# Performance work log

Hardware: AMD Instinct MI355X
Metric: run time of the kernel (lower is better)

The kernel has to match this reference:

```python
import jax, jax.numpy as jnp
import numpy as np

B, S, D, H, L, FF, V, TYPES = 16, 512, 1024, 16, 8, 4096, 30522, 2
DH = D // H
BETA = 1.0          # pbit_temperature
EPS = 1e-12         # layer_norm_eps
STD = 0.02          # initializer_range


def _ln(x, g, b):
    m = x.mean(-1, keepdims=True)
    v = ((x - m) ** 2).mean(-1, keepdims=True)
    return (x - m) * jax.lax.rsqrt(v + EPS) * g + b


def setup_inputs() -> dict:
    key = jax.random.key(0)
    ks = iter(jax.random.split(key, 32))
    rn = lambda shape: (jax.random.normal(next(ks), shape, dtype=jnp.float32) * STD)
    inp = {
        'input_ids': jax.random.randint(next(ks), (B, S), 0, V),
        'token_type_ids': jax.random.randint(next(ks), (B, S), 0, TYPES),
        'tok_emb': rn((V, D)),
        'pos_emb': rn((S, D)),
        'type_emb': rn((TYPES, D)),
        'emb_g': jnp.ones((D,), jnp.float32),
        'emb_b': jnp.zeros((D,), jnp.float32),
        # stacked per-layer parameters [L, ...]
        'Wq': rn((L, D, D)), 'bq': jnp.zeros((L, D), jnp.float32),
        'Wk': rn((L, D, D)), 'bk': jnp.zeros((L, D), jnp.float32),
        'Wv': rn((L, D, D)), 'bv': jnp.zeros((L, D), jnp.float32),
        'Wo': rn((L, D, D)), 'bo': jnp.zeros((L, D), jnp.float32),
        'ln1_g': jnp.ones((L, D), jnp.float32), 'ln1_b': jnp.zeros((L, D), jnp.float32),
        'ln2_g': jnp.ones((L, D), jnp.float32), 'ln2_b': jnp.zeros((L, D), jnp.float32),
        'W1': rn((L, D, FF)), 'b1': jnp.zeros((L, FF), jnp.float32),
        'W2': rn((L, FF, D)), 'b2': jnp.zeros((L, D), jnp.float32),
    }
    return inp


def reference(input_ids, token_type_ids, tok_emb, pos_emb, type_emb, emb_g, emb_b,
              Wq, bq, Wk, bk, Wv, bv, Wo, bo, ln1_g, ln1_b, ln2_g, ln2_b,
              W1, b1, W2, b2):
    # Embeddings (eval mode: TSU noise + dropout are identity)
    h = tok_emb[input_ids] + pos_emb[None, :, :] + type_emb[token_type_ids]
    h = _ln(h, emb_g, emb_b)

    def layer(h, p):
        wq, bq_, wk, bk_, wv, bv_, wo, bo_, g1, bb1, g2, bb2, w1, bf1, w2, bf2 = p
        x = _ln(h, g1, bb1)  # pre-LN per TinyBioBERTLayer
        q = (x @ wq + bq_).reshape(B, S, H, DH)
        k = (x @ wk + bk_).reshape(B, S, H, DH)
        v = (x @ wv + bv_).reshape(B, S, H, DH)
        # P-bit attention in expectation == temperature-scaled softmax SDPA
        scores = jnp.einsum('bqhd,bkhd->bhqk', q, k) * (BETA / np.sqrt(DH))
        a = jax.nn.softmax(scores, axis=-1)
        ctx = jnp.einsum('bhqk,bkhd->bqhd', a, v).reshape(B, S, D)
        h = h + ctx @ wo + bo_
        y = _ln(h, g2, bb2)
        y = jax.nn.gelu(y @ w1 + bf1, approximate=False) @ w2 + bf2
        return h + y, None

    params = (Wq, bq, Wk, bk, Wv, bv, Wo, bo, ln1_g, ln1_b, ln2_g, ln2_b, W1, b1, W2, b2)
    h, _ = jax.lax.scan(layer, h, params)
    return h
```

## Files before the change

kernel.cpp:

```cpp
#include <hip/hip_runtime.h>
#include <math.h>

#define B_  16
#define S_  512
#define D_  1024
#define H_  16
#define DH_ 64
#define L_  8
#define FF_ 4096
#define M_  (B_*S_)

typedef __attribute__((ext_vector_type(4))) float  f32x4;
typedef __attribute__((ext_vector_type(8))) short  s8v;
typedef __attribute__((ext_vector_type(4))) short  s4v;
typedef __attribute__((ext_vector_type(8))) __bf16 bf8v;

__device__ __forceinline__ short f2bf(float f) {
  union { float f; unsigned u; } x; x.f = f;
  unsigned r = x.u + 0x7fffu + ((x.u >> 16) & 1u);
  return (short)(r >> 16);
}

__device__ __forceinline__ f32x4 mfma16(s8v a, s8v b, f32x4 c) {
  return __builtin_amdgcn_mfma_f32_16x16x32_bf16(
      __builtin_bit_cast(bf8v, a), __builtin_bit_cast(bf8v, b), c, 0, 0, 0);
}

__device__ __forceinline__ void gl_lds16(const void* g, void* lds) {
  __builtin_amdgcn_global_load_lds(
      (const __attribute__((address_space(1))) unsigned int*)g,
      (__attribute__((address_space(3))) unsigned int*)lds, 16, 0, 0);
}

__device__ __forceinline__ float gelu_f(float v) {
  const float t  = 0.7978845608f * (v + 0.044715f * v * v * v);
  const float e  = __expf(-2.0f * fabsf(t));
  const float th = copysignf((1.f - e) / (1.f + e), t);
  return 0.5f * v * (1.0f + th);
}

__global__ __launch_bounds__(256) void tcvt(const float* __restrict__ src,
                                            short* __restrict__ dst, int R, int C,
                                            size_t dls) {
  __shared__ float tile[32][33];
  src += (size_t)blockIdx.z * R * C;
  dst += (size_t)blockIdx.z * dls;
  const int c0 = blockIdx.x * 32, r0 = blockIdx.y * 32;
  const int tx = threadIdx.x & 31, ty = threadIdx.x >> 5;
#pragma unroll
  for (int i = 0; i < 32; i += 8)
    tile[ty + i][tx] = src[(size_t)(r0 + ty + i) * C + (c0 + tx)];
  __syncthreads();
#pragma unroll
  for (int i = 0; i < 32; i += 8)
    dst[(size_t)(c0 + ty + i) * R + (r0 + tx)] = f2bf(tile[tx][ty + i]);
}

__global__ __launch_bounds__(256) void embed_ln(
    const int* __restrict__ ids, const int* __restrict__ tts,
    const float* __restrict__ tok, const float* __restrict__ pos,
    const float* __restrict__ typ, const float* __restrict__ g,
    const float* __restrict__ bta, float* __restrict__ h) {
  const int row = blockIdx.x;
  const int s = row & (S_ - 1);
  const int id = ids[row], tt = tts[row];
  const int t = threadIdx.x;
  const float4 a = ((const float4*)(tok + (size_t)id * D_))[t];
  const float4 p = ((const float4*)(pos + (size_t)s  * D_))[t];
  const float4 y = ((const float4*)(typ + (size_t)tt * D_))[t];
  float x0 = a.x + p.x + y.x, x1 = a.y + p.y + y.y;
  float x2 = a.z + p.z + y.z, x3 = a.w + p.w + y.w;
  float sum = x0 + x1 + x2 + x3;
  float sq  = x0*x0 + x1*x1 + x2*x2 + x3*x3;
  __shared__ float red[8];
#pragma unroll
  for (int d = 1; d < 64; d <<= 1) { sum += __shfl_xor(sum, d); sq += __shfl_xor(sq, d); }
  if ((t & 63) == 0) { red[t >> 6] = sum; red[(t >> 6) + 4] = sq; }
  __syncthreads();
  sum = red[0] + red[1] + red[2] + red[3];
  sq  = red[4] + red[5] + red[6] + red[7];
  const float mean = sum * (1.f / D_);
  const float var  = sq * (1.f / D_) - mean * mean;
  const float rstd = rsqrtf(fmaxf(var, 0.f) + 1e-12f);
  const float4 gg = ((const float4*)g)[t];
  const float4 bb = ((const float4*)bta)[t];
  float4 o;
  o.x = (x0 - mean) * rstd * gg.x + bb.x;
  o.y = (x1 - mean) * rstd * gg.y + bb.y;
  o.z = (x2 - mean) * rstd * gg.z + bb.z;
  o.w = (x3 - mean) * rstd * gg.w + bb.w;
  ((float4*)(h + (size_t)row * D_))[t] = o;
}

__global__ __launch_bounds__(256) void ln_bf16(
    const float* __restrict__ h, const float* __restrict__ g,
    const float* __restrict__ bta, short* __restrict__ out) {
  const int row = blockIdx.x;
  const int t = threadIdx.x;
  const float4 x = ((const float4*)(h + (size_t)row * D_))[t];
  float sum = x.x + x.y + x.z + x.w;
  float sq  = x.x*x.x + x.y*x.y + x.z*x.z + x.w*x.w;
  __shared__ float red[8];
#pragma unroll
  for (int d = 1; d < 64; d <<= 1) { sum += __shfl_xor(sum, d); sq += __shfl_xor(sq, d); }
  if ((t & 63) == 0) { red[t >> 6] = sum; red[(t >> 6) + 4] = sq; }
  __syncthreads();
  sum = red[0] + red[1] + red[2] + red[3];
  sq  = red[4] + red[5] + red[6] + red[7];
  const float mean = sum * (1.f / D_);
  const float var  = sq * (1.f / D_) - mean * mean;
  const float rstd = rsqrtf(fmaxf(var, 0.f) + 1e-12f);
  const float4 gg = ((const float4*)g)[t];
  const float4 bb = ((const float4*)bta)[t];
  s4v o;
  o[0] = f2bf((x.x - mean) * rstd * gg.x + bb.x);
  o[1] = f2bf((x.y - mean) * rstd * gg.y + bb.y);
  o[2] = f2bf((x.z - mean) * rstd * gg.z + bb.z);
  o[3] = f2bf((x.w - mean) * rstd * gg.w + bb.w);
  *(s4v*)&out[(size_t)row * D_ + t * 4] = o;
}

__global__ __launch_bounds__(256) void ln_red(
    float* __restrict__ h, const float* __restrict__ p0,
    const float* __restrict__ p1, const float* __restrict__ badd,
    const float* __restrict__ g, const float* __restrict__ bta,
    short* __restrict__ out) {
  const int row = blockIdx.x;
  const int t = threadIdx.x;
  const size_t off = (size_t)row * D_;
  float4 x = ((const float4*)(h + off))[t];
  const float4 a = ((const float4*)(p0 + off))[t];
  const float4 b = ((const float4*)(p1 + off))[t];
  const float4 c = ((const float4*)badd)[t];
  x.x += a.x + b.x + c.x; x.y += a.y + b.y + c.y;
  x.z += a.z + b.z + c.z; x.w += a.w + b.w + c.w;
  ((float4*)(h + off))[t] = x;
  float sum = x.x + x.y + x.z + x.w;
  float sq  = x.x*x.x + x.y*x.y + x.z*x.z + x.w*x.w;
  __shared__ float red[8];
#pragma unroll
  for (int d = 1; d < 64; d <<= 1) { sum += __shfl_xor(sum, d); sq += __shfl_xor(sq, d); }
  if ((t & 63) == 0) { red[t >> 6] = sum; red[(t >> 6) + 4] = sq; }
  __syncthreads();
  sum = red[0] + red[1] + red[2] + red[3];
  sq  = red[4] + red[5] + red[6] + red[7];
  const float mean = sum * (1.f / D_);
  const float var  = sq * (1.f / D_) - mean * mean;
  const float rstd = rsqrtf(fmaxf(var, 0.f) + 1e-12f);
  const float4 gg = ((const float4*)g)[t];
  const float4 bb = ((const float4*)bta)[t];
  s4v o;
  o[0] = f2bf((x.x - mean) * rstd * gg.x + bb.x);
  o[1] = f2bf((x.y - mean) * rstd * gg.y + bb.y);
  o[2] = f2bf((x.z - mean) * rstd * gg.z + bb.z);
  o[3] = f2bf((x.w - mean) * rstd * gg.w + bb.w);
  *(s4v*)&out[off + t * 4] = o;
}

__global__ __launch_bounds__(256) void final_add(
    float* __restrict__ h, const float* __restrict__ p0,
    const float* __restrict__ p1, const float* __restrict__ badd) {
  const int row = blockIdx.x;
  const int t = threadIdx.x;
  const size_t off = (size_t)row * D_;
  float4 x = ((const float4*)(h + off))[t];
  const float4 a = ((const float4*)(p0 + off))[t];
  const float4 b = ((const float4*)(p1 + off))[t];
  const float4 c = ((const float4*)badd)[t];
  x.x += a.x + b.x + c.x; x.y += a.y + b.y + c.y;
  x.z += a.z + b.z + c.z; x.w += a.w + b.w + c.w;
  ((float4*)(h + off))[t] = x;
}

template<int MODE>
__global__ __launch_bounds__(512, 1) void gemm8(
    const short* __restrict__ A, const short* __restrict__ Bt,
    const float* __restrict__ b0, const float* __restrict__ b1,
    const float* __restrict__ b2, short* __restrict__ out,
    float* __restrict__ hres, int N, int K, int LD, int nby) {
  __shared__ __align__(16) char lds[131072];
  const int tid = threadIdx.x, wid = tid >> 6, lane = tid & 63;
  const int wr = wid >> 2, wc = wid & 3;
  const int l15 = lane & 15, l4 = lane >> 4;

  const int n8 = (int)gridDim.x >> 3;
  const int bid = (int)blockIdx.x;
  const int xcd = bid & 7, tt_ = bid >> 3;
  const int nbv = (MODE == 4) ? nby * 2 : nby;
  const int cpx = n8 / nbv;
  const int bx = xcd * cpx + tt_ / nbv;
  const int bv = tt_ % nbv;
  const int by = (MODE == 4) ? (bv & 3) : bv;
  const int slice = (MODE == 4) ? (bv >> 2) : 0;
  const int which = (MODE == 6) ? (by >> 2) : 0;

  const short* __restrict__ Ab = A + (size_t)bx * 256 * LD + (size_t)slice * K;
  const short* __restrict__ Bb = Bt + (size_t)by * 256 * LD + (size_t)slice * K;

  const int str0 = tid >> 3;
  const int stc  = (((tid & 7) ^ (str0 & 7)) * 8);
  const int r7  = l15 & 7;
  const int kx0 = ((l4) ^ r7) * 16;
  const int kx1 = ((4 + l4) ^ r7) * 16;
  const int arow = (wr * 128 + l15) * 128;
  const int brow = (wc * 64 + l15) * 128;

  f32x4 acc[8][4];
#pragma unroll
  for (int m = 0; m < 8; ++m)
#pragma unroll
    for (int n = 0; n < 4; ++n) acc[m][n] = f32x4{0.f, 0.f, 0.f, 0.f};
  s8v af[8][2], bf[4][2];

  const int nt = K >> 6, it = nt >> 1;

#define BAR_ __builtin_amdgcn_s_barrier()
#define LGKM0_ asm volatile("s_waitcnt lgkmcnt(0)" ::: "memory")
#define VMC_(n) asm volatile("s_waitcnt vmcnt(" #n ")" ::: "memory")
#define ST_(isB, slot, hh, kt) do { \
    const short* _g = ((isB) ? Bb : Ab) + (size_t)((hh) * 128 + str0) * LD + ((kt) << 6) + stc; \
    char* _d = lds + ((isB) ? 65536 : 0) + (slot) * 32768 + (hh) * 16384 + wid * 1024; \
    gl_lds16(_g, _d); \
    gl_lds16(_g + (size_t)64 * LD, _d + 8192); \
  } while (0)
#define RDA4_(slot, g) do { \
    const char* _p = lds + (slot) * 32768 + arow + (g) * 8192; \
    _Pragma("unroll") for (int _i = 0; _i < 4; ++_i) { \
      af[(g)*4+_i][0] = *(const s8v*)(_p + _i * 2048 + kx0); \
      af[(g)*4+_i][1] = *(const s8v*)(_p + _i * 2048 + kx1); } \
  } while (0)
#define RDB2_(slot, g) do { \
    const char* _p = lds + 65536 + (slot) * 32768 + brow + (g) * 4096; \
    _Pragma("unroll") for (int _i = 0; _i < 2; ++_i) { \
      bf[(g)*2+_i][0] = *(const s8v*)(_p + _i * 2048 + kx0); \
      bf[(g)*2+_i][1] = *(const s8v*)(_p + _i * 2048 + kx1); } \
  } while (0)
#define MM_S(mq, nq) do { \
    __builtin_amdgcn_s_setprio(1); \
    _Pragma("unroll") for (int _mf = 0; _mf < 4; ++_mf) \
    _Pragma("unroll") for (int _nf = 0; _nf < 2; ++_nf) \
    _Pragma("unroll") for (int _ks = 0; _ks < 2; ++_ks) \
      acc[(mq)*4+_mf][(nq)*2+_nf] = \
        mfma16(bf[(nq)*2+_nf][_ks], af[(mq)*4+_mf][_ks], acc[(mq)*4+_mf][(nq)*2+_nf]); \
    __builtin_amdgcn_s_setprio(0); \
  } while (0)
#define MM_U(mq, nq) do { \
    __builtin_amdgcn_s_setprio(1); \
    _Pragma("unroll") for (int _mf = 0; _mf < 4; ++_mf) \
    _Pragma("unroll") for (int _nf = 0; _nf < 2; ++_nf) \
    _Pragma("unroll") for (int _ks = 0; _ks < 2; ++_ks) \
      acc[(mq)*4+_mf][(nq)*2+_nf] = \
        mfma16(af[(mq)*4+_mf][_ks], bf[(nq)*2+_nf][_ks], acc[(mq)*4+_mf][(nq)*2+_nf]); \
    __builtin_amdgcn_s_setprio(0); \
  } while (0)
#define KLOOP_(MMX) \
  for (int t = 0; t < it; ++t) { \
    const int ka = 2 * t, kb = ka + 1; \
    const bool s2 = (ka + 2) < nt, s3 = (kb + 2) < nt; \
    RDA4_(0, 0); RDB2_(0, 0); \
    ST_(1, 1, 1, kb); \
    BAR_; LGKM0_; MMX(0, 0); BAR_; \
    RDB2_(0, 1); \
    BAR_; LGKM0_; MMX(0, 1); BAR_; \
    RDA4_(0, 1); \
    if (s2) ST_(1, 0, 0, ka + 2); \
    BAR_; LGKM0_; MMX(1, 0); BAR_; \
    if (s2) { ST_(1, 0, 1, ka + 2); VMC_(4); } else { VMC_(0); } \
    BAR_; MMX(1, 1); BAR_; \
    RDA4_(1, 0); RDB2_(1, 0); \
    if (s2) ST_(0, 0, 0, ka + 2); \
    BAR_; LGKM0_; MMX(0, 0); BAR_; \
    RDB2_(1, 1); \
    if (s2) ST_(0, 0, 1, ka + 2); \
    BAR_; LGKM0_; MMX(0, 1); BAR_; \
    RDA4_(1, 1); \
    if (s3) ST_(1, 1, 0, kb + 2); \
    BAR_; LGKM0_; MMX(1, 0); BAR_; \
    if (s3) { ST_(0, 1, 0, kb + 2); ST_(0, 1, 1, kb + 2); VMC_(6); } \
    BAR_; MMX(1, 1); BAR_; \
  }

  ST_(1,0,0,0); ST_(1,0,1,0); ST_(0,0,0,0); ST_(0,0,1,0);
  ST_(1,1,0,1); ST_(0,1,0,1); ST_(0,1,1,1);
  VMC_(6);
  BAR_;

  if (MODE == 6 && which == 2) { KLOOP_(MM_U); }
  else                         { KLOOP_(MM_S); }

  const int r0 = bx * 256 + wr * 128;
  const int c0 = by * 256 + wc * 64;
  if (MODE == 6 && which == 2) {
    short* __restrict__ vout = out + 2 * (size_t)M_ * D_;
#pragma unroll
    for (int n = 0; n < 4; ++n) {
      const int col = c0 + n * 16 + l15;
      const int colw = col & (D_ - 1);
      const int hd = colw >> 6, dh = colw & 63;
      const float bb = b2[colw];
#pragma unroll
      for (int m = 0; m < 8; ++m) {
        const int row = r0 + m * 16 + l4 * 4;
        const int b = row >> 9, s = row & 511;
        s4v pk;
#pragma unroll
        for (int rr = 0; rr < 4; ++rr) pk[rr] = f2bf(acc[m][n][rr] + bb);
        *(s4v*)&vout[(((size_t)(b * H_ + hd) * DH_) + dh) * S_ + s] = pk;
      }
    }
    return;
  }
  const float* __restrict__ bias = (MODE == 6) ? (which == 0 ? b0 : b1) : b0;
  short* __restrict__ outw = (MODE == 6) ? out + (size_t)which * M_ * D_ : out;
  float* __restrict__ pp =
      (MODE == 4) ? hres + (size_t)slice * ((size_t)M_ * D_) : hres;

  float4 bb4[4];
#pragma unroll
  for (int n = 0; n < 4; ++n) {
    const int colb = c0 + n * 16 + l4 * 4;
    const int colw = colb & (D_ - 1);
    bb4[n] = float4{0.f, 0.f, 0.f, 0.f};
    if (MODE == 6)              bb4[n] = *(const float4*)&bias[colw];
    else if (MODE != 4 && bias) bb4[n] = *(const float4*)&bias[colb];
  }
#pragma unroll
  for (int m = 0; m < 8; ++m) {
    const int row = r0 + m * 16 + l15;
#pragma unroll
    for (int n = 0; n < 4; ++n) {
      const int colb = c0 + n * 16 + l4 * 4;
      const int colw = colb & (D_ - 1);
      float v0 = acc[m][n][0] + bb4[n].x, v1 = acc[m][n][1] + bb4[n].y;
      float v2 = acc[m][n][2] + bb4[n].z, v3 = acc[m][n][3] + bb4[n].w;
      if (MODE == 2) {
        float4* hp = (float4*)&hres[(size_t)row * N + colb];
        float4 hv = *hp;
        hv.x += v0; hv.y += v1; hv.z += v2; hv.w += v3;
        *hp = hv;
      } else if (MODE == 4) {
        float4 pv; pv.x = v0; pv.y = v1; pv.z = v2; pv.w = v3;
        *(float4*)&pp[(size_t)row * N + colb] = pv;
      } else {
        if (MODE == 1) { v0 = gelu_f(v0); v1 = gelu_f(v1); v2 = gelu_f(v2); v3 = gelu_f(v3); }
        s4v pk;
        pk[0] = f2bf(v0); pk[1] = f2bf(v1); pk[2] = f2bf(v2); pk[3] = f2bf(v3);
        if (MODE == 6) {
          const int b = row >> 9, s = row & 511, hd = colw >> 6, dh = colw & 63;
          *(s4v*)&outw[((((size_t)b * H_ + hd) * S_ + s) << 6) + dh] = pk;
        } else {
          *(s4v*)&outw[(size_t)row * N + colb] = pk;
        }
      }
    }
  }
#undef BAR_
#undef LGKM0_
#undef VMC_
#undef ST_
#undef RDA4_
#undef RDB2_
#undef MM_S
#undef MM_U
#undef KLOOP_
}

__global__ __launch_bounds__(256, 4) void attn(
    const short* __restrict__ Q, const short* __restrict__ K,
    const short* __restrict__ Vt, short* __restrict__ ctx) {
  __shared__ __align__(16) short Kl[64 * 72];
  __shared__ __align__(16) short Vl[64 * 72];
  __shared__ __align__(16) short Pl[4][32 * 72];

  const int tid = threadIdx.x, wid = tid >> 6, lane = tid & 63;
  const int l15 = lane & 15, l4 = lane >> 4;
  const int bid = (int)blockIdx.x;
  const int xcd = bid & 7, idx = bid >> 3;
  const int bh   = xcd * 32 + (idx >> 2);
  const int qblk = idx & 3;
  const short* Qb = Q  + (size_t)bh * S_ * DH_;
  const short* Kb = K  + (size_t)bh * S_ * DH_;
  const short* Vb = Vt + (size_t)bh * DH_ * S_;

  const int qoff = qblk * 128 + wid * 32;

  s8v qf[2][2];
#pragma unroll
  for (int mf = 0; mf < 2; ++mf)
#pragma unroll
    for (int ks = 0; ks < 2; ++ks)
      qf[mf][ks] = *(const s8v*)&Qb[(size_t)(qoff + mf * 16 + l15) * DH_ + ks * 32 + l4 * 8];

  f32x4 o[2][4];
  float rm[2][4], rs[2][4];
#pragma unroll
  for (int mf = 0; mf < 2; ++mf) {
#pragma unroll
    for (int nf = 0; nf < 4; ++nf) o[mf][nf] = f32x4{0.f, 0.f, 0.f, 0.f};
#pragma unroll
    for (int r = 0; r < 4; ++r) { rm[mf][r] = -1e30f; rs[mf][r] = 0.f; }
  }

  const int srow = tid >> 3;
  const int sch  = (tid & 7) * 8;

  s8v rk[2], rv[2];
#pragma unroll
  for (int r = 0; r < 2; ++r) {
    rk[r] = *(const s8v*)&Kb[(size_t)(srow + r * 32) * DH_ + sch];
    rv[r] = *(const s8v*)&Vb[(size_t)(srow + r * 32) * S_ + sch];
  }

  for (int kt = 0; kt < S_ / 64; ++kt) {
    __syncthreads();
#pragma unroll
    for (int r = 0; r < 2; ++r) {
      *(s8v*)&Kl[(srow + r * 32) * 72 + sch] = rk[r];
      *(s8v*)&Vl[(srow + r * 32) * 72 + sch] = rv[r];
    }
    __syncthreads();
    if (kt + 1 < S_ / 64) {
#pragma unroll
      for (int r = 0; r < 2; ++r) {
        rk[r] = *(const s8v*)&Kb[(size_t)((kt + 1) * 64 + srow + r * 32) * DH_ + sch];
        rv[r] = *(const s8v*)&Vb[(size_t)(srow + r * 32) * S_ + (kt + 1) * 64 + sch];
      }
    }

    f32x4 sc[2][4];
#pragma unroll
    for (int mf = 0; mf < 2; ++mf)
#pragma unroll
      for (int nt = 0; nt < 4; ++nt) sc[mf][nt] = f32x4{0.f, 0.f, 0.f, 0.f};
    __builtin_amdgcn_s_setprio(1);
#pragma unroll
    for (int nt = 0; nt < 4; ++nt)
#pragma unroll
      for (int ks = 0; ks < 2; ++ks) {
        const s8v kf = *(const s8v*)&Kl[(nt * 16 + l15) * 72 + ks * 32 + l4 * 8];
#pragma unroll
        for (int mf = 0; mf < 2; ++mf)
          sc[mf][nt] = mfma16(qf[mf][ks], kf, sc[mf][nt]);
      }
    __builtin_amdgcn_s_setprio(0);

#pragma unroll
    for (int mf = 0; mf < 2; ++mf) {
      float tm[4];
#pragma unroll
      for (int r = 0; r < 4; ++r) {
        sc[mf][0][r] *= 0.125f; sc[mf][1][r] *= 0.125f;
        sc[mf][2][r] *= 0.125f; sc[mf][3][r] *= 0.125f;
        tm[r] = fmaxf(fmaxf(sc[mf][0][r], sc[mf][1][r]),
                      fmaxf(sc[mf][2][r], sc[mf][3][r]));
      }
#pragma unroll
      for (int d = 1; d < 16; d <<= 1)
#pragma unroll
        for (int r = 0; r < 4; ++r) tm[r] = fmaxf(tm[r], __shfl_xor(tm[r], d));
      float ps[4];
#pragma unroll
      for (int r = 0; r < 4; ++r) {
        const float nm = fmaxf(rm[mf][r], tm[r]);
        const float so = __expf(rm[mf][r] - nm);
        rm[mf][r] = nm;
        rs[mf][r] *= so;
#pragma unroll
        for (int nf = 0; nf < 4; ++nf) o[mf][nf][r] *= so;
        float psum = 0.f;
#pragma unroll
        for (int nt = 0; nt < 4; ++nt) {
          const float pv = __expf(sc[mf][nt][r] - nm);
          sc[mf][nt][r] = pv;
          psum += pv;
        }
        ps[r] = psum;
      }
#pragma unroll
      for (int d = 1; d < 16; d <<= 1)
#pragma unroll
        for (int r = 0; r < 4; ++r) ps[r] += __shfl_xor(ps[r], d);
#pragma unroll
      for (int r = 0; r < 4; ++r) rs[mf][r] += ps[r];
#pragma unroll
      for (int nt = 0; nt < 4; ++nt)
#pragma unroll
        for (int r = 0; r < 4; ++r)
          Pl[wid][(mf * 16 + l4 * 4 + r) * 72 + nt * 16 + l15] = f2bf(sc[mf][nt][r]);
    }
    asm volatile("s_waitcnt lgkmcnt(0)" ::: "memory");

    __builtin_amdgcn_s_setprio(1);
#pragma unroll
    for (int ks = 0; ks < 2; ++ks) {
      s8v pf[2], vf[4];
#pragma unroll
      for (int mf = 0; mf < 2; ++mf)
        pf[mf] = *(const s8v*)&Pl[wid][(mf * 16 + l15) * 72 + ks * 32 + l4 * 8];
#pragma unroll
      for (int nf = 0; nf < 4; ++nf)
        vf[nf] = *(const s8v*)&Vl[(nf * 16 + l15) * 72 + ks * 32 + l4 * 8];
#pragma unroll
      for (int mf = 0; mf < 2; ++mf)
#pragma unroll
        for (int nf = 0; nf < 4; ++nf)
          o[mf][nf] = mfma16(pf[mf], vf[nf], o[mf][nf]);
    }
    __builtin_amdgcn_s_setprio(0);
  }

  const int bb = bh >> 4, hh = bh & 15;
#pragma unroll
  for (int mf = 0; mf < 2; ++mf)
#pragma unroll
    for (int r = 0; r < 4; ++r) {
      const int qrow = qoff + mf * 16 + l4 * 4 + r;
      const float inv = 1.0f / rs[mf][r];
      short* dst = ctx + (size_t)(bb * S_ + qrow) * D_ + hh * DH_;
#pragma unroll
      for (int nf = 0; nf < 4; ++nf)
        dst[nf * 16 + l15] = f2bf(o[mf][nf][r] * inv);
    }
}

extern "C" void kernel_launch(void* const* d_in, const int* in_sizes, int n_in,
                              void* d_out, int out_size, void* d_ws, size_t ws_size,
                              hipStream_t stream) {
  const int*   ids = (const int*)d_in[0];
  const int*   tts = (const int*)d_in[1];
  const float* tok = (const float*)d_in[2];
  const float* pos = (const float*)d_in[3];
  const float* typ = (const float*)d_in[4];
  const float* eg  = (const float*)d_in[5];
  const float* eb  = (const float*)d_in[6];
  const float* Wq  = (const float*)d_in[7];  const float* bq = (const float*)d_in[8];
  const float* Wk  = (const float*)d_in[9];  const float* bk = (const float*)d_in[10];
  const float* Wv  = (const float*)d_in[11]; const float* bv = (const float*)d_in[12];
  const float* Wo  = (const float*)d_in[13]; const float* bo = (const float*)d_in[14];
  const float* g1  = (const float*)d_in[15]; const float* be1 = (const float*)d_in[16];
  const float* g2  = (const float*)d_in[17]; const float* be2 = (const float*)d_in[18];
  const float* W1  = (const float*)d_in[19]; const float* b1 = (const float*)d_in[20];
  const float* W2  = (const float*)d_in[21]; const float* b2 = (const float*)d_in[22];

  float* h = (float*)d_out;

  const size_t szDD  = (size_t)D_ * D_;
  const size_t szDF  = (size_t)D_ * FF_;
  const size_t xb_b  = (size_t)M_ * D_ * 2;
  const size_t big_b = (size_t)M_ * FF_ * 2;
  const size_t pa_b  = (size_t)M_ * D_ * 4;
  const size_t wfull = (szDD * 4 + szDF * 2) * 2 * L_;
  const bool full = ws_size >= wfull + xb_b + big_b + 8192;
  const bool sk   = ws_size >= wfull + xb_b + big_b + 2 * pa_b + 8192;

  char* p = (char*)d_ws;
  auto alloc = [&](size_t bytes) { char* r = p; p += (bytes + 255) & ~(size_t)255; return r; };
  const size_t wl = full ? L_ : 1;
  short* wqkvT = (short*)alloc(szDD * 3 * 2 * wl);
  short* woT   = (short*)alloc(szDD * 2 * wl);
  short* w1T   = (short*)alloc(szDF * 2 * wl);
  short* w2T   = (short*)alloc(szDF * 2 * wl);
  short* xb  = (short*)alloc(xb_b);
  char*  big = alloc(big_b);
  float* pa0 = sk ? (float*)alloc(pa_b) : nullptr;
  float* pa1 = sk ? (float*)alloc(pa_b) : nullptr;
  short* qb  = (short*)big;
  short* vb  = (short*)(big + 2 * xb_b);
  short* cb  = xb;
  short* tb  = (short*)big;

  if (full) {
    tcvt<<<dim3(D_/32,  D_/32,  L_), 256, 0, stream>>>(Wq, wqkvT,          D_,  D_,  3*szDD);
    tcvt<<<dim3(D_/32,  D_/32,  L_), 256, 0, stream>>>(Wk, wqkvT +   szDD, D_,  D_,  3*szDD);
    tcvt<<<dim3(D_/32,  D_/32,  L_), 256, 0, stream>>>(Wv, wqkvT + 2*szDD, D_,  D_,  3*szDD);
    tcvt<<<dim3(D_/32,  D_/32,  L_), 256, 0, stream>>>(Wo, woT, D_,  D_,  szDD);
    tcvt<<<dim3(FF_/32, D_/32,  L_), 256, 0, stream>>>(W1, w1T, D_,  FF_, szDF);
    tcvt<<<dim3(D_/32,  FF_/32, L_), 256, 0, stream>>>(W2, w2T, FF_, D_,  szDF);
  }

  embed_ln<<<M_, 256, 0, stream>>>(ids, tts, tok, pos, typ, eg, eb, h);

  const int nbx = M_ / 256;
  for (int l = 0; l < L_; ++l) {
    if (!full) {
      tcvt<<<dim3(D_/32,  D_/32,  1), 256, 0, stream>>>(Wq + (size_t)l*szDD, wqkvT,          D_,  D_,  0);
      tcvt<<<dim3(D_/32,  D_/32,  1), 256, 0, stream>>>(Wk + (size_t)l*szDD, wqkvT +   szDD, D_,  D_,  0);
      tcvt<<<dim3(D_/32,  D_/32,  1), 256, 0, stream>>>(Wv + (size_t)l*szDD, wqkvT + 2*szDD, D_,  D_,  0);
      tcvt<<<dim3(D_/32,  D_/32,  1), 256, 0, stream>>>(Wo + (size_t)l*szDD, woT, D_,  D_,  0);
      tcvt<<<dim3(FF_/32, D_/32,  1), 256, 0, stream>>>(W1 + (size_t)l*szDF, w1T, D_,  FF_, 0);
      tcvt<<<dim3(D_/32,  FF_/32, 1), 256, 0, stream>>>(W2 + (size_t)l*szDF, w2T, FF_, D_,  0);
    }
    const size_t o3 = full ? (size_t)l * 3 * szDD : 0;
    const size_t od = full ? (size_t)l * szDD : 0;
    const size_t of = full ? (size_t)l * szDF : 0;

    if (l == 0 || !sk)
      ln_bf16<<<M_, 256, 0, stream>>>(h, g1 + l*D_, be1 + l*D_, xb);
    else
      ln_red<<<M_, 256, 0, stream>>>(h, pa0, pa1, b2 + (l-1)*D_,
                                     g1 + l*D_, be1 + l*D_, xb);

    gemm8<6><<<nbx * (3*D_/256), 512, 0, stream>>>(
        xb, wqkvT + o3, bq + l*D_, bk + l*D_, bv + l*D_, qb, nullptr, 3*D_, D_, D_, 3*D_/256);

    attn<<<(S_/128) * B_ * H_, 256, 0, stream>>>(
        qb, qb + (size_t)M_*D_, vb, cb);

    if (sk) {
      gemm8<4><<<nbx * (D_/256) * 2, 512, 0, stream>>>(
          cb, woT + od, nullptr, nullptr, nullptr, nullptr, pa0, D_, D_/2, D_, D_/256);
      ln_red<<<M_, 256, 0, stream>>>(h, pa0, pa1, bo + l*D_,
                                     g2 + l*D_, be2 + l*D_, xb);
    } else {
      gemm8<2><<<nbx * (D_/256), 512, 0, stream>>>(
          cb, woT + od, bo + l*D_, nullptr, nullptr, nullptr, h, D_, D_, D_, D_/256);
      ln_bf16<<<M_, 256, 0, stream>>>(h, g2 + l*D_, be2 + l*D_, xb);
    }

    gemm8<1><<<nbx * (FF_/256), 512, 0, stream>>>(
        xb, w1T + of, b1 + l*FF_, nullptr, nullptr, tb, nullptr, FF_, D_, D_, FF_/256);

    if (sk) {
      gemm8<4><<<nbx * (D_/256) * 2, 512, 0, stream>>>(
          tb, w2T + of, nullptr, nullptr, nullptr, nullptr, pa0, D_, FF_/2, FF_, D_/256);
    } else {
      gemm8<2><<<nbx * (D_/256), 512, 0, stream>>>(
          tb, w2T + of, b2 + l*D_, nullptr, nullptr, nullptr, h, D_, FF_, FF_, D_/256);
    }
  }
  if (sk)
    final_add<<<M_, 256, 0, stream>>>(h, pa0, pa1, b2 + (L_-1)*D_);
}
```

Baseline: 3.006 ms.

## Switch GEMM to 4 waves with 128x128 per-wave tiles

Reworks the 256x256-tile bf16 GEMM from 8 waves (2x4, 128x64 per wave) to 4 waves (2x2, 128x128 per wave). Each wave now holds 64 accumulator fragments and reuses every A and B fragment read from LDS across more MFMAs, which cuts LDS read traffic per FLOP. Each thread issues twice as many global-to-LDS loads, and the vmcnt waits and the pipeline schedule are adjusted to match. The cost is much higher register pressure (256 accumulator VGPRs plus operands), possible spills, and half as many waves per CU to hide latency.

Measured after the change: 3.965 ms. 1.32x slower.

```diff
diff --git a/kernel.cpp b/kernel.cpp
--- a/kernel.cpp
+++ b/kernel.cpp
@@ -173,14 +173,14 @@
 }
 
 template<int MODE>
-__global__ __launch_bounds__(512, 1) void gemm8(
+__global__ __launch_bounds__(256, 1) void gemm8(
     const short* __restrict__ A, const short* __restrict__ Bt,
     const float* __restrict__ b0, const float* __restrict__ b1,
     const float* __restrict__ b2, short* __restrict__ out,
     float* __restrict__ hres, int N, int K, int LD, int nby) {
   __shared__ __align__(16) char lds[131072];
   const int tid = threadIdx.x, wid = tid >> 6, lane = tid & 63;
-  const int wr = wid >> 2, wc = wid & 3;
+  const int wr = wid >> 1, wc = wid & 1;
   const int l15 = lane & 15, l4 = lane >> 4;
 
   const int n8 = (int)gridDim.x >> 3;
@@ -203,14 +203,14 @@
   const int kx0 = ((l4) ^ r7) * 16;
   const int kx1 = ((4 + l4) ^ r7) * 16;
   const int arow = (wr * 128 + l15) * 128;
-  const int brow = (wc * 64 + l15) * 128;
-
-  f32x4 acc[8][4];
+  const int brow = (wc * 128 + l15) * 128;
+
+  f32x4 acc[8][8];
 #pragma unroll
   for (int m = 0; m < 8; ++m)
 #pragma unroll
-    for (int n = 0; n < 4; ++n) acc[m][n] = f32x4{0.f, 0.f, 0.f, 0.f};
-  s8v af[8][2], bf[4][2];
+    for (int n = 0; n < 8; ++n) acc[m][n] = f32x4{0.f, 0.f, 0.f, 0.f};
+  s8v af[8][2], bfA[4][2], bfB[4][2];
 
   const int nt = K >> 6, it = nt >> 1;
 
@@ -221,7 +221,9 @@
     const short* _g = ((isB) ? Bb : Ab) + (size_t)((hh) * 128 + str0) * LD + ((kt) << 6) + stc; \
     char* _d = lds + ((isB) ? 65536 : 0) + (slot) * 32768 + (hh) * 16384 + wid * 1024; \
     gl_lds16(_g, _d); \
+    gl_lds16(_g + (size_t)32 * LD, _d + 4096); \
     gl_lds16(_g + (size_t)64 * LD, _d + 8192); \
+    gl_lds16(_g + (size_t)96 * LD, _d + 12288); \
   } while (0)
 #define RDA4_(slot, g) do { \
     const char* _p = lds + (slot) * 32768 + arow + (g) * 8192; \
@@ -229,71 +231,69 @@
       af[(g)*4+_i][0] = *(const s8v*)(_p + _i * 2048 + kx0); \
       af[(g)*4+_i][1] = *(const s8v*)(_p + _i * 2048 + kx1); } \
   } while (0)
-#define RDB2_(slot, g) do { \
-    const char* _p = lds + 65536 + (slot) * 32768 + brow + (g) * 4096; \
-    _Pragma("unroll") for (int _i = 0; _i < 2; ++_i) { \
-      bf[(g)*2+_i][0] = *(const s8v*)(_p + _i * 2048 + kx0); \
-      bf[(g)*2+_i][1] = *(const s8v*)(_p + _i * 2048 + kx1); } \
+#define RDB4_(slot, g, DST) do { \
+    const char* _p = lds + 65536 + (slot) * 32768 + brow + (g) * 8192; \
+    _Pragma("unroll") for (int _i = 0; _i < 4; ++_i) { \
+      DST[_i][0] = *(const s8v*)(_p + _i * 2048 + kx0); \
+      DST[_i][1] = *(const s8v*)(_p + _i * 2048 + kx1); } \
   } while (0)
-#define MM_S(mq, nq) do { \
+#define MM_S(aq, BF, bq) do { \
     __builtin_amdgcn_s_setprio(1); \
     _Pragma("unroll") for (int _mf = 0; _mf < 4; ++_mf) \
-    _Pragma("unroll") for (int _nf = 0; _nf < 2; ++_nf) \
+    _Pragma("unroll") for (int _nf = 0; _nf < 4; ++_nf) \
     _Pragma("unroll") for (int _ks = 0; _ks < 2; ++_ks) \
-      acc[(mq)*4+_mf][(nq)*2+_nf] = \
-        mfma16(bf[(nq)*2+_nf][_ks], af[(mq)*4+_mf][_ks], acc[(mq)*4+_mf][(nq)*2+_nf]); \
+      acc[(aq)*4+_mf][(bq)*4+_nf] = \
+        mfma16(BF[_nf][_ks], af[(aq)*4+_mf][_ks], acc[(aq)*4+_mf][(bq)*4+_nf]); \
     __builtin_amdgcn_s_setprio(0); \
   } while (0)
-#define MM_U(mq, nq) do { \
+#define MM_U(aq, BF, bq) do { \
     __builtin_amdgcn_s_setprio(1); \
     _Pragma("unroll") for (int _mf = 0; _mf < 4; ++_mf) \
-    _Pragma("unroll") for (int _nf = 0; _nf < 2; ++_nf) \
+    _Pragma("unroll") for (int _nf = 0; _nf < 4; ++_nf) \
     _Pragma("unroll") for (int _ks = 0; _ks < 2; ++_ks) \
-      acc[(mq)*4+_mf][(nq)*2+_nf] = \
-        mfma16(af[(mq)*4+_mf][_ks], bf[(nq)*2+_nf][_ks], acc[(mq)*4+_mf][(nq)*2+_nf]); \
+      acc[(aq)*4+_mf][(bq)*4+_nf] = \
+        mfma16(af[(aq)*4+_mf][_ks], BF[_nf][_ks], acc[(aq)*4+_mf][(bq)*4+_nf]); \
     __builtin_amdgcn_s_setprio(0); \
   } while (0)
 #define KLOOP_(MMX) \
   for (int t = 0; t < it; ++t) { \
     const int ka = 2 * t, kb = ka + 1; \
     const bool s2 = (ka + 2) < nt, s3 = (kb + 2) < nt; \
-    RDA4_(0, 0); RDB2_(0, 0); \
+    RDA4_(0, 0); RDA4_(0, 1); RDB4_(0, 0, bfA); \
     ST_(1, 1, 1, kb); \
-    BAR_; LGKM0_; MMX(0, 0); BAR_; \
-    RDB2_(0, 1); \
-    BAR_; LGKM0_; MMX(0, 1); BAR_; \
-    RDA4_(0, 1); \
+    BAR_; LGKM0_; MMX(0, bfA, 0); BAR_; \
+    RDB4_(0, 1, bfB); \
+    BAR_; LGKM0_; MMX(1, bfA, 0); BAR_; \
     if (s2) ST_(1, 0, 0, ka + 2); \
-    BAR_; LGKM0_; MMX(1, 0); BAR_; \
-    if (s2) { ST_(1, 0, 1, ka + 2); VMC_(4); } else { VMC_(0); } \
-    BAR_; MMX(1, 1); BAR_; \
-    RDA4_(1, 0); RDB2_(1, 0); \
+    BAR_; MMX(0, bfB, 1); BAR_; \
+    if (s2) { ST_(1, 0, 1, ka + 2); VMC_(8); } else { VMC_(0); } \
+    BAR_; MMX(1, bfB, 1); BAR_; \
+    RDA4_(1, 0); RDA4_(1, 1); RDB4_(1, 0, bfA); \
     if (s2) ST_(0, 0, 0, ka + 2); \
-    BAR_; LGKM0_; MMX(0, 0); BAR_; \
-    RDB2_(1, 1); \
+    BAR_; LGKM0_; MMX(0, bfA, 0); BAR_; \
+    RDB4_(1, 1, bfB); \
     if (s2) ST_(0, 0, 1, ka + 2); \
-    BAR_; LGKM0_; MMX(0, 1); BAR_; \
-    RDA4_(1, 1); \
+    BAR_; LGKM0_; MMX(1, bfA, 0); BAR_; \
     if (s3) ST_(1, 1, 0, kb + 2); \
-    BAR_; LGKM0_; MMX(1, 0); BAR_; \
-    if (s3) { ST_(0, 1, 0, kb + 2); ST_(0, 1, 1, kb + 2); VMC_(6); } \
-    BAR_; MMX(1, 1); BAR_; \
+    BAR_; MMX(0, bfB, 1); BAR_; \
+    if (s3) { ST_(0, 1, 0, kb + 2); ST_(0, 1, 1, kb + 2); VMC_(12); } \
+    BAR_; MMX(1, bfB, 1); BAR_; \
   }
 
   ST_(1,0,0,0); ST_(1,0,1,0); ST_(0,0,0,0); ST_(0,0,1,0);
   ST_(1,1,0,1); ST_(0,1,0,1); ST_(0,1,1,1);
-  VMC_(6);
+  VMC_(12);
   BAR_;
 
   if (MODE == 6 && which == 2) { KLOOP_(MM_U); }
   else                         { KLOOP_(MM_S); }
 
   const int r0 = bx * 256 + wr * 128;
-  const int c0 = by * 256 + wc * 64;
+  const int c0 = by * 256 + wc * 128;
   if (MODE == 6 && which == 2) {
     short* __restrict__ vout = out + 2 * (size_t)M_ * D_;
 #pragma unroll
-    for (int n = 0; n < 4; ++n) {
+    for (int n = 0; n < 8; ++n) {
       const int col = c0 + n * 16 + l15;
       const int colw = col & (D_ - 1);
       const int hd = colw >> 6, dh = colw & 63;
@@ -315,9 +315,9 @@
   float* __restrict__ pp =
       (MODE == 4) ? hres + (size_t)slice * ((size_t)M_ * D_) : hres;
 
-  float4 bb4[4];
-#pragma unroll
-  for (int n = 0; n < 4; ++n) {
+  float4 bb4[8];
+#pragma unroll
+  for (int n = 0; n < 8; ++n) {
     const int colb = c0 + n * 16 + l4 * 4;
     const int colw = colb & (D_ - 1);
     bb4[n] = float4{0.f, 0.f, 0.f, 0.f};
@@ -328,7 +328,7 @@
   for (int m = 0; m < 8; ++m) {
     const int row = r0 + m * 16 + l15;
 #pragma unroll
-    for (int n = 0; n < 4; ++n) {
+    for (int n = 0; n < 8; ++n) {
       const int colb = c0 + n * 16 + l4 * 4;
       const int colw = colb & (D_ - 1);
       float v0 = acc[m][n][0] + bb4[n].x, v1 = acc[m][n][1] + bb4[n].y;
@@ -359,7 +359,7 @@
 #undef VMC_
 #undef ST_
 #undef RDA4_
-#undef RDB2_
+#undef RDB4_
 #undef MM_S
 #undef MM_U
 #undef KLOOP_
@@ -600,31 +600,31 @@
       ln_red<<<M_, 256, 0, stream>>>(h, pa0, pa1, b2 + (l-1)*D_,
                                      g1 + l*D_, be1 + l*D_, xb);
 
-    gemm8<6><<<nbx * (3*D_/256), 512, 0, stream>>>(
+    gemm8<6><<<nbx * (3*D_/256), 256, 0, stream>>>(
         xb, wqkvT + o3, bq + l*D_, bk + l*D_, bv + l*D_, qb, nullptr, 3*D_, D_, D_, 3*D_/256);
 
     attn<<<(S_/128) * B_ * H_, 256, 0, stream>>>(
         qb, qb + (size_t)M_*D_, vb, cb);
 
     if (sk) {
-      gemm8<4><<<nbx * (D_/256) * 2, 512, 0, stream>>>(
+      gemm8<4><<<nbx * (D_/256) * 2, 256, 0, stream>>>(
           cb, woT + od, nullptr, nullptr, nullptr, nullptr, pa0, D_, D_/2, D_, D_/256);
       ln_red<<<M_, 256, 0, stream>>>(h, pa0, pa1, bo + l*D_,
                                      g2 + l*D_, be2 + l*D_, xb);
     } else {
-      gemm8<2><<<nbx * (D_/256), 512, 0, stream>>>(
+      gemm8<2><<<nbx * (D_/256), 256, 0, stream>>>(
           cb, woT + od, bo + l*D_, nullptr, nullptr, nullptr, h, D_, D_, D_, D_/256);
       ln_bf16<<<M_, 256, 0, stream>>>(h, g2 + l*D_, be2 + l*D_, xb);
     }
 
-    gemm8<1><<<nbx * (FF_/256), 512, 0, stream>>>(
+    gemm8<1><<<nbx * (FF_/256), 256, 0, stream>>>(
         xb, w1T + of, b1 + l*FF_, nullptr, nullptr, tb, nullptr, FF_, D_, D_, FF_/256);
 
     if (sk) {
-      gemm8<4><<<nbx * (D_/256) * 2, 512, 0, stream>>>(
+      gemm8<4><<<nbx * (D_/256) * 2, 256, 0, stream>>>(
           tb, w2T + of, nullptr, nullptr, nullptr, nullptr, pa0, D_, FF_/2, FF_, D_/256);
     } else {
-      gemm8<2><<<nbx * (D_/256), 512, 0, stream>>>(
+      gemm8<2><<<nbx * (D_/256), 256, 0, stream>>>(
           tb, w2T + of, b2 + l*D_, nullptr, nullptr, nullptr, h, D_, FF_, FF_, D_/256);
     }
   }
```
